# Performance work log

Measured on AMD Instinct MI355X. Metric: run time of the kernel, lower is better.

Reference implementation:

```python
import jax, jax.numpy as jnp
import numpy as np

D_MODEL = 1024
N_HEADS = 16
D_K = 64

def setup_inputs() -> dict:
    key = jax.random.key(0)
    k0, k1, k2, k3, k4 = jax.random.split(key, 5)
    B, S = 4, 4096
    std = 0.02
    x = jax.random.normal(k0, (B, S, D_MODEL), dtype=jnp.float32)
    # nn.Linear weights are [out, in]; init normal(0, 0.02) as in _init_weights
    W_q = std * jax.random.normal(k1, (N_HEADS * D_K, D_MODEL), dtype=jnp.float32)
    W_k = std * jax.random.normal(k2, (N_HEADS * D_K, D_MODEL), dtype=jnp.float32)
    W_v = std * jax.random.normal(k3, (N_HEADS * D_K, D_MODEL), dtype=jnp.float32)
    W_o = std * jax.random.normal(k4, (D_MODEL, N_HEADS * D_K), dtype=jnp.float32)
    return {"x": x, "W_q": W_q, "W_k": W_k, "W_v": W_v, "W_o": W_o}

def reference(x, W_q, W_k, W_v, W_o):
    B, S, _ = x.shape
    H, Dk = N_HEADS, D_K
    # projections (nn.Linear: x @ W.T), reshape to [B, S, H, Dk]
    q = (x @ W_q.T).reshape(B, S, H, Dk)
    k = (x @ W_k.T).reshape(B, S, H, Dk)
    v = (x @ W_v.T).reshape(B, S, H, Dk)
    scale = 1.0 / jnp.sqrt(jnp.float32(Dk))
    # No softmax between the two matmuls -> reassociate (QK^T)V = Q(K^TV),
    # identical math, O(S*d^2) instead of O(S^2*d).
    kv = jnp.einsum('bshd,bshe->bhde', k, v)          # [B, H, Dk, Dk]
    attn = jnp.einsum('bshd,bhde->bshe', q, kv) * scale  # [B, S, H, Dk]
    out = attn.reshape(B, S, H * Dk) @ W_o.T
    return out
```

## Files before the change

kernel.cpp:

```cpp
#include <hip/hip_runtime.h>
#include <hip/hip_bf16.h>
#include <cstdint>


typedef __bf16 bf16x8 __attribute__((ext_vector_type(8)));
typedef float f32x4 __attribute__((ext_vector_type(4)));
typedef unsigned short ushort_t;

__device__ inline void gld_lds16(const void* g, void* l) {
    __builtin_amdgcn_global_load_lds(
        (const __attribute__((address_space(1))) unsigned int*)g,
        (__attribute__((address_space(3))) unsigned int*)l,
        16, 0, 0);
}

__device__ inline ushort_t f2bf(float f) {
    uint32_t u = __float_as_uint(f);
    uint32_t r = (u + 0x7fffu + ((u >> 16) & 1u)) >> 16;
    return (ushort_t)r;
}
__device__ inline float bf2f(ushort_t u) {
    return __uint_as_float((uint32_t)u << 16);
}

template <typename OutT>
__global__ __launch_bounds__(256, 2)
void gemm_bt(const ushort_t* __restrict__ A, int lda, long strideA,
             const ushort_t* __restrict__ B, int ldb, long strideB,
             OutT* __restrict__ C0, int ldc0, long strideC0, int K)
{
    __shared__ ushort_t lA[128 * 32];
    __shared__ ushort_t lB[128 * 32];

    const int t    = threadIdx.x;
    const int lane = t & 63;
    const int wid  = t >> 6;
    const int z    = blockIdx.z;

    A += (size_t)z * strideA;
    B += (size_t)z * strideB;

    const int m0 = blockIdx.x * 128;
    const int n0 = blockIdx.y * 128;

    const int wm = (wid >> 1) * 64;
    const int wn = (wid & 1) * 64;
    const int mr = lane & 15;
    const int q4 = lane >> 4;

    const int row_a = t >> 2;
    const int seg   = ((t & 3) ^ ((t >> 3) & 3)) * 8;
    const int csw   = (q4 ^ ((mr >> 1) & 3)) * 16;

    f32x4 acc[4][4] = {};

    for (int k0 = 0; k0 < K; k0 += 32) {
        __syncthreads();
        gld_lds16(A + (size_t)(m0 + row_a) * lda + k0 + seg,      (char*)lA + wid * 1024);
        gld_lds16(A + (size_t)(m0 + 64 + row_a) * lda + k0 + seg, (char*)lA + 4096 + wid * 1024);
        gld_lds16(B + (size_t)(n0 + row_a) * ldb + k0 + seg,      (char*)lB + wid * 1024);
        gld_lds16(B + (size_t)(n0 + 64 + row_a) * ldb + k0 + seg, (char*)lB + 4096 + wid * 1024);
        __syncthreads();

        bf16x8 af[4], bf[4];
#pragma unroll
        for (int i = 0; i < 4; ++i)
            af[i] = *(const bf16x8*)((const char*)lA + (wm + i * 16 + mr) * 64 + csw);
#pragma unroll
        for (int j = 0; j < 4; ++j)
            bf[j] = *(const bf16x8*)((const char*)lB + (wn + j * 16 + mr) * 64 + csw);
#pragma unroll
        for (int i = 0; i < 4; ++i)
#pragma unroll
            for (int j = 0; j < 4; ++j)
                acc[i][j] = __builtin_amdgcn_mfma_f32_16x16x32_bf16(af[i], bf[j], acc[i][j], 0, 0, 0);
    }

    OutT* Cw = C0 + (size_t)z * strideC0;
#pragma unroll
    for (int i = 0; i < 4; ++i) {
        const int rbase = m0 + wm + i * 16 + q4 * 4;
#pragma unroll
        for (int j = 0; j < 4; ++j) {
            const int col = n0 + wn + j * 16 + mr;
#pragma unroll
            for (int r = 0; r < 4; ++r) {
                const float v = acc[i][j][r];
                const size_t off = (size_t)(rbase + r) * ldc0 + col;
                if constexpr (sizeof(OutT) == 2) Cw[off] = f2bf(v);
                else                             Cw[off] = v;
            }
        }
    }
}

__global__ __launch_bounds__(256, 2)
void gemm_gram(const ushort_t* __restrict__ X, ushort_t* __restrict__ Gp)
{
    __shared__ ushort_t lA[128 * 32];
    __shared__ ushort_t lB[128 * 32];

    const int t    = threadIdx.x;
    const int lane = t & 63;
    const int wid  = t >> 6;

    const int z  = blockIdx.x;
    const int bb = z >> 2, ks = z & 3;

    int ti = 0, rem = blockIdx.y;
    while (rem >= 8 - ti) { rem -= 8 - ti; ++ti; }
    const int tj = ti + rem;
    const int m0 = ti * 128;
    const int n0 = tj * 128;

    const ushort_t* A = X + (size_t)bb * 4096 + (size_t)ks * 1024;

    const int wm = (wid >> 1) * 64;
    const int wn = (wid & 1) * 64;
    const int mr = lane & 15;
    const int q4 = lane >> 4;

    const int row_a = t >> 2;
    const int seg   = ((t & 3) ^ ((t >> 3) & 3)) * 8;
    const int csw   = (q4 ^ ((mr >> 1) & 3)) * 16;

    f32x4 acc[4][4] = {};

    for (int k0 = 0; k0 < 1024; k0 += 32) {
        __syncthreads();
        gld_lds16(A + (size_t)(m0 + row_a) * 16384 + k0 + seg,      (char*)lA + wid * 1024);
        gld_lds16(A + (size_t)(m0 + 64 + row_a) * 16384 + k0 + seg, (char*)lA + 4096 + wid * 1024);
        gld_lds16(A + (size_t)(n0 + row_a) * 16384 + k0 + seg,      (char*)lB + wid * 1024);
        gld_lds16(A + (size_t)(n0 + 64 + row_a) * 16384 + k0 + seg, (char*)lB + 4096 + wid * 1024);
        __syncthreads();

        bf16x8 af[4], bf[4];
#pragma unroll
        for (int i = 0; i < 4; ++i)
            af[i] = *(const bf16x8*)((const char*)lA + (wm + i * 16 + mr) * 64 + csw);
#pragma unroll
        for (int j = 0; j < 4; ++j)
            bf[j] = *(const bf16x8*)((const char*)lB + (wn + j * 16 + mr) * 64 + csw);
#pragma unroll
        for (int i = 0; i < 4; ++i)
#pragma unroll
            for (int j = 0; j < 4; ++j)
                acc[i][j] = __builtin_amdgcn_mfma_f32_16x16x32_bf16(af[i], bf[j], acc[i][j], 0, 0, 0);
    }

    ushort_t* Cw = Gp + ((size_t)z << 20);
#pragma unroll
    for (int i = 0; i < 4; ++i) {
        const int rbase = m0 + wm + i * 16 + q4 * 4;
#pragma unroll
        for (int j = 0; j < 4; ++j) {
            const int col = n0 + wn + j * 16 + mr;
#pragma unroll
            for (int r = 0; r < 4; ++r)
                Cw[(size_t)(rbase + r) * 1024 + col] = f2bf(acc[i][j][r]);
        }
    }
}

__global__ __launch_bounds__(256)
void reduce_g_t(const ushort_t* __restrict__ Gp, ushort_t* __restrict__ G)
{
    __shared__ float acc[64 * 65];

    const int t  = threadIdx.x;
    const int b  = blockIdx.y;
    const int tr = blockIdx.x >> 4, tc = blockIdx.x & 15;
    const int sr = (tr <= tc) ? tr : tc;
    const int sc = (tr <= tc) ? tc : tr;
    const bool flip = tr > tc;

#pragma unroll
    for (int p = 0; p < 4; ++p) {
        const int idx = p * 256 + t;
        const int r = idx >> 4, c = (idx & 15) * 4;
        float a0 = 0.f, a1 = 0.f, a2 = 0.f, a3 = 0.f;
#pragma unroll
        for (int ksl = 0; ksl < 4; ++ksl) {
            const ushort4 u = *(const ushort4*)&Gp[((size_t)(b * 4 + ksl) << 20)
                                                   + (size_t)(sr * 64 + r) * 1024 + sc * 64 + c];
            a0 += bf2f(u.x); a1 += bf2f(u.y); a2 += bf2f(u.z); a3 += bf2f(u.w);
        }
        acc[r * 65 + c + 0] = a0;
        acc[r * 65 + c + 1] = a1;
        acc[r * 65 + c + 2] = a2;
        acc[r * 65 + c + 3] = a3;
    }
    __syncthreads();

#pragma unroll
    for (int p = 0; p < 4; ++p) {
        const int idx = p * 256 + t;
        const int r = idx >> 4, c = (idx & 15) * 4;
        float v0, v1, v2, v3;
        if (flip) {
            v0 = acc[(c + 0) * 65 + r];
            v1 = acc[(c + 1) * 65 + r];
            v2 = acc[(c + 2) * 65 + r];
            v3 = acc[(c + 3) * 65 + r];
        } else {
            v0 = acc[r * 65 + c + 0];
            v1 = acc[r * 65 + c + 1];
            v2 = acc[r * 65 + c + 2];
            v3 = acc[r * 65 + c + 3];
        }
        ushort4 o;
        o.x = f2bf(v0); o.y = f2bf(v1); o.z = f2bf(v2); o.w = f2bf(v3);
        *(ushort4*)&G[((size_t)b << 20) + (size_t)(tr * 64 + r) * 1024 + tc * 64 + c] = o;
    }
}

__global__ __launch_bounds__(256)
void cast_x_t(const float* __restrict__ x, ushort_t* __restrict__ xb,
              ushort_t* __restrict__ xbT)
{
    __shared__ ushort_t lt[64 * 66];
    const int t  = threadIdx.x;
    const int s0 = blockIdx.x * 64;
    const int i0 = blockIdx.y * 64;

#pragma unroll
    for (int c = 0; c < 4; ++c) {
        const int idx = c * 256 + t;
        const int r = idx >> 4, c4 = (idx & 15) * 4;
        const float4 f = *(const float4*)&x[(size_t)(s0 + r) * 1024 + i0 + c4];
        ushort4 o;
        o.x = f2bf(f.x); o.y = f2bf(f.y); o.z = f2bf(f.z); o.w = f2bf(f.w);
        *(ushort4*)&xb[(size_t)(s0 + r) * 1024 + i0 + c4] = o;
        *(uint32_t*)&lt[r * 66 + c4]     = (uint32_t)o.x | ((uint32_t)o.y << 16);
        *(uint32_t*)&lt[r * 66 + c4 + 2] = (uint32_t)o.z | ((uint32_t)o.w << 16);
    }
    __syncthreads();
#pragma unroll
    for (int c = 0; c < 4; ++c) {
        const int idx = c * 256 + t;
        const int ri = idx >> 4, s4 = (idx & 15) * 4;
        ushort4 o;
        o.x = lt[(s4 + 0) * 66 + ri];
        o.y = lt[(s4 + 1) * 66 + ri];
        o.z = lt[(s4 + 2) * 66 + ri];
        o.w = lt[(s4 + 3) * 66 + ri];
        *(ushort4*)&xbT[(size_t)(i0 + ri) * 16384 + s0 + s4] = o;
    }
}

__global__ __launch_bounds__(256)
void cast_wt(const float* __restrict__ W, ushort_t* __restrict__ WT)
{
    __shared__ ushort_t lt[64 * 66];
    const int t  = threadIdx.x;
    const int r0 = blockIdx.x * 64;
    const int c0 = blockIdx.y * 64;

#pragma unroll
    for (int c = 0; c < 4; ++c) {
        const int idx = c * 256 + t;
        const int r = idx >> 4, c4 = (idx & 15) * 4;
        const float4 f = *(const float4*)&W[(size_t)(r0 + r) * 1024 + c0 + c4];
        ushort4 o;
        o.x = f2bf(f.x); o.y = f2bf(f.y); o.z = f2bf(f.z); o.w = f2bf(f.w);
        *(uint32_t*)&lt[r * 66 + c4]     = (uint32_t)o.x | ((uint32_t)o.y << 16);
        *(uint32_t*)&lt[r * 66 + c4 + 2] = (uint32_t)o.z | ((uint32_t)o.w << 16);
    }
    __syncthreads();
#pragma unroll
    for (int c = 0; c < 4; ++c) {
        const int idx = c * 256 + t;
        const int ri = idx >> 4, s4 = (idx & 15) * 4;
        ushort4 o;
        o.x = lt[(s4 + 0) * 66 + ri];
        o.y = lt[(s4 + 1) * 66 + ri];
        o.z = lt[(s4 + 2) * 66 + ri];
        o.w = lt[(s4 + 3) * 66 + ri];
        *(ushort4*)&WT[(size_t)(c0 + ri) * 1024 + r0 + s4] = o;
    }
}

__global__ __launch_bounds__(256)
void cast_w2(const float* __restrict__ a, const float* __restrict__ b,
             ushort_t* __restrict__ out)
{
    const float* src = (blockIdx.y == 0) ? a : b;
    const int i = (blockIdx.x * 256 + threadIdx.x) * 4;
    const float4 f = *(const float4*)&src[i];
    ushort4 o;
    o.x = f2bf(f.x); o.y = f2bf(f.y); o.z = f2bf(f.z); o.w = f2bf(f.w);
    *(ushort4*)&out[(size_t)blockIdx.y * 1048576 + i] = o;
}

__global__ __launch_bounds__(256)
void kvblk(const ushort_t* __restrict__ H, const ushort_t* __restrict__ Wv,
           float* __restrict__ KVp)
{
    __shared__ ushort_t sH[64 * 132];
    __shared__ ushort_t sV[64 * 132];

    const int t  = threadIdx.x;
    const int is = blockIdx.x;
    const int bh = blockIdx.y;
    const int b  = bh >> 4, h = bh & 15;

    const ushort_t* Hp = H + ((size_t)b << 20) + (size_t)(h * 64) * 1024 + is * 128;
    const ushort_t* Vp = Wv + (size_t)(h * 64) * 1024 + is * 128;

#pragma unroll
    for (int i2 = 0; i2 < 8; ++i2) {
        const int ci = i2 * 256 + t;
        const int r = ci >> 5, c = (ci & 31) * 4;
        *(uint2*)&sH[r * 132 + c] = *(const uint2*)&Hp[(size_t)r * 1024 + c];
        *(uint2*)&sV[r * 132 + c] = *(const uint2*)&Vp[(size_t)r * 1024 + c];
    }
    __syncthreads();

    const int d0 = (t >> 4) * 4;
    const int e0 = (t & 15) * 4;
    float acc[4][4] = {};

#pragma unroll 2
    for (int i4 = 0; i4 < 128; i4 += 4) {
        uint2 hu[4], vu[4];
#pragma unroll
        for (int j = 0; j < 4; ++j) {
            hu[j] = *(const uint2*)&sH[(d0 + j) * 132 + i4];
            vu[j] = *(const uint2*)&sV[(e0 + j) * 132 + i4];
        }
        float hf[4][4], vf[4][4];
#pragma unroll
        for (int j = 0; j < 4; ++j) {
            hf[j][0] = __uint_as_float(hu[j].x << 16);
            hf[j][1] = __uint_as_float(hu[j].x & 0xffff0000u);
            hf[j][2] = __uint_as_float(hu[j].y << 16);
            hf[j][3] = __uint_as_float(hu[j].y & 0xffff0000u);
            vf[j][0] = __uint_as_float(vu[j].x << 16);
            vf[j][1] = __uint_as_float(vu[j].x & 0xffff0000u);
            vf[j][2] = __uint_as_float(vu[j].y << 16);
            vf[j][3] = __uint_as_float(vu[j].y & 0xffff0000u);
        }
#pragma unroll
        for (int ii = 0; ii < 4; ++ii)
#pragma unroll
            for (int di = 0; di < 4; ++di)
#pragma unroll
                for (int ej = 0; ej < 4; ++ej)
                    acc[di][ej] += hf[di][ii] * vf[ej][ii];
    }

    float* outp = KVp + ((size_t)(is * 64 + bh)) * 4096;
#pragma unroll
    for (int i = 0; i < 4; ++i) {
        float4 o; o.x = acc[i][0]; o.y = acc[i][1]; o.z = acc[i][2]; o.w = acc[i][3];
        *(float4*)&outp[(d0 + i) * 64 + e0] = o;
    }
}

__global__ __launch_bounds__(256)
void reduce_kv8(const float4* __restrict__ in, float4* __restrict__ out)
{
    const int i = blockIdx.x * 256 + threadIdx.x;
    float4 a = in[i];
#pragma unroll
    for (int s = 1; s < 8; ++s) {
        const float4 b = in[s * 65536 + i];
        a.x += b.x; a.y += b.y; a.z += b.z; a.w += b.w;
    }
    out[i] = a;
}

__global__ __launch_bounds__(256)
void make_E(const float* __restrict__ KV, const float* __restrict__ Wo,
            ushort_t* __restrict__ Et)
{
    __shared__ float skv[64 * 65];
    __shared__ float swo[64 * 65];

    const int t  = threadIdx.x;
    const int bh = blockIdx.y;
    const int b  = bh >> 4, h = bh & 15;
    const int j0 = blockIdx.x * 64;

    const float* kvp = KV + (size_t)bh * 4096;
#pragma unroll
    for (int i = 0; i < 4; ++i) {
        const int idx = t + i * 256;
        const int r = idx >> 4, c = (idx & 15) * 4;
        const float4 f = *(const float4*)&kvp[r * 64 + c];
        skv[r * 65 + c + 0] = f.x;
        skv[r * 65 + c + 1] = f.y;
        skv[r * 65 + c + 2] = f.z;
        skv[r * 65 + c + 3] = f.w;
        const float4 g = *(const float4*)&Wo[(size_t)(j0 + r) * 1024 + h * 64 + c];
        swo[r * 65 + c + 0] = g.x;
        swo[r * 65 + c + 1] = g.y;
        swo[r * 65 + c + 2] = g.z;
        swo[r * 65 + c + 3] = g.w;
    }
    __syncthreads();

    const int d0 = (t & 15) * 4;
#pragma unroll
    for (int pass = 0; pass < 4; ++pass) {
        const int jloc = (t >> 4) + pass * 16;
        float s0 = 0.f, s1 = 0.f, s2 = 0.f, s3 = 0.f;
        const float* wrow = &swo[jloc * 65];
#pragma unroll 8
        for (int e = 0; e < 64; ++e) {
            const float w = wrow[e];
            s0 += skv[(d0 + 0) * 65 + e] * w;
            s1 += skv[(d0 + 1) * 65 + e] * w;
            s2 += skv[(d0 + 2) * 65 + e] * w;
            s3 += skv[(d0 + 3) * 65 + e] * w;
        }
        ushort4 o;
        o.x = f2bf(s0 * 0.125f);
        o.y = f2bf(s1 * 0.125f);
        o.z = f2bf(s2 * 0.125f);
        o.w = f2bf(s3 * 0.125f);
        *(ushort4*)&Et[((size_t)b * 1024 + j0 + jloc) * 1024 + h * 64 + d0] = o;
    }
}


extern "C" void kernel_launch(void* const* d_in, const int* in_sizes, int n_in,
                              void* d_out, int out_size, void* d_ws, size_t ws_size,
                              hipStream_t stream)
{
    const float* x  = (const float*)d_in[0];
    const float* Wq = (const float*)d_in[1];
    const float* Wk = (const float*)d_in[2];
    const float* Wv = (const float*)d_in[3];
    const float* Wo = (const float*)d_in[4];
    float* out = (float*)d_out;

    const int B = 4, S = 4096, D = 1024;
    const long MB1 = 1048576;

    char* ws = (char*)d_ws;
    size_t off = 0;
    auto alloc = [&](size_t bytes) -> void* {
        void* p = ws + off;
        off += (bytes + 255) & ~(size_t)255;
        return p;
    };
    ushort_t* xb   = (ushort_t*)alloc((size_t)B * S * D * 2);
    ushort_t* xbT  = (ushort_t*)alloc((size_t)D * B * S * 2);
    ushort_t* wkv  = (ushort_t*)alloc((size_t)2 * D * D * 2);
    ushort_t* wqT  = (ushort_t*)alloc((size_t)D * D * 2);
    ushort_t* Gb   = (ushort_t*)alloc((size_t)B * D * D * 2);
    float*    kvp  = (float*)alloc((size_t)8 * 64 * 4096 * 4);
    float*    kvr  = (float*)alloc((size_t)64 * 4096 * 4);
    ushort_t* Fb   = (ushort_t*)alloc((size_t)B * D * D * 2);
    char*     R1   = (char*)alloc((size_t)16 * MB1 * 2);
    ushort_t* Gp = (ushort_t*)R1;
    ushort_t* Hb = (ushort_t*)R1;
    ushort_t* Et = (ushort_t*)(R1 + 8 * MB1 * 2);
    ushort_t* wkb = wkv;
    ushort_t* wvb = wkv + MB1;

    cast_x_t<<<dim3(256, 16), dim3(256), 0, stream>>>(x, xb, xbT);
    cast_w2<<<dim3(1024, 2), dim3(256), 0, stream>>>(Wk, Wv, wkv);
    cast_wt<<<dim3(16, 16), dim3(256), 0, stream>>>(Wq, wqT);

    gemm_gram<<<dim3(16, 36), dim3(256), 0, stream>>>(xbT, Gp);
    reduce_g_t<<<dim3(256, 4), dim3(256), 0, stream>>>(Gp, Gb);

    gemm_bt<ushort_t><<<dim3(8, 8, 4), dim3(256), 0, stream>>>(
        wkb, D, 0, Gb, D, MB1, Hb, D, MB1, D);

    kvblk<<<dim3(8, 64), dim3(256), 0, stream>>>(Hb, wvb, kvp);
    reduce_kv8<<<dim3(256), dim3(256), 0, stream>>>((const float4*)kvp, (float4*)kvr);

    make_E<<<dim3(16, 64), dim3(256), 0, stream>>>(kvr, Wo, Et);

    gemm_bt<ushort_t><<<dim3(8, 8, 4), dim3(256), 0, stream>>>(
        Et, D, MB1, wqT, D, 0, Fb, D, (long)D * D, D);

    gemm_bt<float><<<dim3(32, 8, 4), dim3(256), 0, stream>>>(
        xb, D, (long)S * D, Fb, D, (long)D * D, out, D, (long)S * D, D);
}
```

Measured before the change: 315.9 us.

## Add 256x256-tile pipelined GEMM kernel for the final output projection

Replaces the 128x128-tile final GEMM (x @ F per batch, fp32 output) with a new 512-thread kernel using 256x256 tiles, 64-wide K steps, double-buffered LDS fed by direct global-to-LDS loads, XOR-swizzled layout, and staging interleaved with MFMA phases under manual waitcnt/barrier control. The larger tile raises arithmetic intensity and cuts global/LDS traffic per flop, and the interleaved prefetch is meant to hide load latency. The cost is 128KB of LDS per block, which limits occupancy. Only 256 blocks are launched, so part of the GPU may sit idle.

Measured after the change: 307.8 us. 2.6% less time.

```diff
diff --git a/kernel.cpp b/kernel.cpp
--- a/kernel.cpp
+++ b/kernel.cpp
@@ -90,6 +90,124 @@
                 if constexpr (sizeof(OutT) == 2) Cw[off] = f2bf(v);
                 else                             Cw[off] = v;
             }
+        }
+    }
+}
+
+__global__ __launch_bounds__(512, 2)
+void gemm256_bt(const ushort_t* __restrict__ A, int lda, long strideA,
+                const ushort_t* __restrict__ B, int ldb, long strideB,
+                float* __restrict__ C, int ldc, long strideC, int K)
+{
+    __shared__ char lds[131072];
+
+    const int t    = threadIdx.x;
+    const int lane = t & 63;
+    const int wid  = t >> 6;
+    const int z    = blockIdx.z;
+
+    A += (size_t)z * strideA;
+    B += (size_t)z * strideB;
+
+    const int m0 = blockIdx.x * 256;
+    const int n0 = blockIdx.y * 256;
+
+    const int wm = wid >> 2;
+    const int wn = wid & 3;
+    const int mr = lane & 15;
+    const int q4 = lane >> 4;
+
+    const int NT = K >> 6;
+
+    const int srow = t >> 3;
+    const int scol = ((t & 7) << 3) ^ (((t >> 3) & 7) << 3);
+
+    auto stage_half = [&](const ushort_t* __restrict__ src, int ld, int org,
+                          int h, int tgt, int bsel) {
+        if (tgt >= NT) return;
+        char* base = lds + bsel + ((tgt & 1) << 15) + (h << 14) + wid * 1024;
+        const ushort_t* g = src + (size_t)(org + h * 128 + srow) * ld + tgt * 64 + scol;
+        gld_lds16(g, base);
+        gld_lds16(g + ((size_t)ld << 6), base + 8192);
+    };
+    auto stage_unit = [&](int u, int tgt) {
+        if (u < 2) stage_half(B, ldb, n0, u,     tgt, 65536);
+        else       stage_half(A, lda, m0, u - 2, tgt, 0);
+    };
+
+    stage_unit(0, 0); stage_unit(1, 0); stage_unit(2, 0); stage_unit(3, 0);
+    stage_unit(0, 1); stage_unit(1, 1); stage_unit(2, 1);
+    asm volatile("s_waitcnt vmcnt(6)" ::: "memory");
+    __builtin_amdgcn_s_barrier();
+
+    f32x4 acc[8][4] = {};
+
+    for (int kt = 0; kt < NT; ++kt) {
+        const char* aBuf = lds + ((kt & 1) << 15) + (wm << 14);
+        const char* bBuf = lds + 65536 + ((kt & 1) << 15) + ((wn >> 1) << 14);
+        const int cb = (wn & 1) << 6;
+
+        bf16x8 bB[4][2];
+#pragma unroll
+        for (int p = 0; p < 4; ++p) {
+            bf16x8 aA[2][2];
+#pragma unroll
+            for (int s = 0; s < 2; ++s) {
+                const int lr = (2 * p + s) * 16 + mr;
+                const int kx = (lr & 7) << 4;
+#pragma unroll
+                for (int ks = 0; ks < 2; ++ks)
+                    aA[s][ks] = *(const bf16x8*)(aBuf + lr * 128 + ((ks * 64 + q4 * 16) ^ kx));
+            }
+            if (p == 0) {
+#pragma unroll
+                for (int j = 0; j < 4; ++j) {
+                    const int c  = cb + j * 16 + mr;
+                    const int kx = (c & 7) << 4;
+#pragma unroll
+                    for (int ks = 0; ks < 2; ++ks)
+                        bB[j][ks] = *(const bf16x8*)(bBuf + c * 128 + ((ks * 64 + q4 * 16) ^ kx));
+                }
+            }
+            if      (p == 0) stage_unit(3, kt + 1);
+            else if (p == 1) stage_unit(0, kt + 2);
+            else if (p == 2) stage_unit(1, kt + 2);
+            else             stage_unit(2, kt + 2);
+
+            __builtin_amdgcn_s_barrier();
+            asm volatile("s_waitcnt lgkmcnt(0)" ::: "memory");
+            __builtin_amdgcn_sched_barrier(0);
+
+            __builtin_amdgcn_s_setprio(1);
+#pragma unroll
+            for (int s = 0; s < 2; ++s)
+#pragma unroll
+                for (int j = 0; j < 4; ++j)
+#pragma unroll
+                    for (int ks = 0; ks < 2; ++ks)
+                        acc[2 * p + s][j] = __builtin_amdgcn_mfma_f32_16x16x32_bf16(
+                            aA[s][ks], bB[j][ks], acc[2 * p + s][j], 0, 0, 0);
+            __builtin_amdgcn_s_setprio(0);
+            __builtin_amdgcn_sched_barrier(0);
+
+            if (p == 3) {
+                if (kt == NT - 2)     asm volatile("s_waitcnt vmcnt(0)" ::: "memory");
+                else if (kt < NT - 2) asm volatile("s_waitcnt vmcnt(6)" ::: "memory");
+            }
+            __builtin_amdgcn_s_barrier();
+        }
+    }
+
+    float* Cw = C + (size_t)z * strideC;
+#pragma unroll
+    for (int i = 0; i < 8; ++i) {
+        const int row = m0 + wm * 128 + i * 16 + q4 * 4;
+#pragma unroll
+        for (int j = 0; j < 4; ++j) {
+            const int col = n0 + wn * 64 + j * 16 + mr;
+#pragma unroll
+            for (int r = 0; r < 4; ++r)
+                Cw[(size_t)(row + r) * ldc + col] = acc[i][j][r];
         }
     }
 }
@@ -478,6 +596,6 @@
     gemm_bt<ushort_t><<<dim3(8, 8, 4), dim3(256), 0, stream>>>(
         Et, D, MB1, wqT, D, 0, Fb, D, (long)D * D, D);
 
-    gemm_bt<float><<<dim3(32, 8, 4), dim3(256), 0, stream>>>(
+    gemm256_bt<<<dim3(16, 4, 4), dim3(512), 0, stream>>>(
         xb, D, (long)S * D, Fb, D, (long)D * D, out, D, (long)S * D, D);
 }
```

## Triple-buffer LDS pipelines for gram and final GEMMs, halve N tile for mid GEMMs

Applied to the files above, without the earlier changes.

Replaces the synchronous load-then-compute loops of the gram GEMM and the final output GEMM with a 3-stage LDS ring. Global-to-LDS loads are issued two tiles ahead and gated by vmcnt waits plus raw barriers, with setprio around the MFMA block. The final GEMM moves to a 256x128 tile with 8x4 accumulators per wave to raise reuse. The two 1024x1024 batched GEMMs switch to 128x64 tiles so the grid has twice as many blocks for better CU occupancy. The cost is more LDS and register pressure and hand-managed wait counts that must match the number of loads issued per stage.

Result: no change. 313.9 us (-0.6%).

```diff
diff --git a/kernel.cpp b/kernel.cpp
--- a/kernel.cpp
+++ b/kernel.cpp
@@ -24,13 +24,13 @@
 }
 
 template <typename OutT>
-__global__ __launch_bounds__(256, 2)
-void gemm_bt(const ushort_t* __restrict__ A, int lda, long strideA,
-             const ushort_t* __restrict__ B, int ldb, long strideB,
-             OutT* __restrict__ C0, int ldc0, long strideC0, int K)
+__global__ __launch_bounds__(256, 4)
+void gemm_bt_n64(const ushort_t* __restrict__ A, int lda, long strideA,
+                 const ushort_t* __restrict__ B, int ldb, long strideB,
+                 OutT* __restrict__ C0, int ldc0, long strideC0, int K)
 {
     __shared__ ushort_t lA[128 * 32];
-    __shared__ ushort_t lB[128 * 32];
+    __shared__ ushort_t lB[64 * 32];
 
     const int t    = threadIdx.x;
     const int lane = t & 63;
@@ -41,10 +41,10 @@
     B += (size_t)z * strideB;
 
     const int m0 = blockIdx.x * 128;
-    const int n0 = blockIdx.y * 128;
+    const int n0 = blockIdx.y * 64;
 
     const int wm = (wid >> 1) * 64;
-    const int wn = (wid & 1) * 64;
+    const int wn = (wid & 1) * 32;
     const int mr = lane & 15;
     const int q4 = lane >> 4;
 
@@ -52,27 +52,26 @@
     const int seg   = ((t & 3) ^ ((t >> 3) & 3)) * 8;
     const int csw   = (q4 ^ ((mr >> 1) & 3)) * 16;
 
-    f32x4 acc[4][4] = {};
+    f32x4 acc[4][2] = {};
 
     for (int k0 = 0; k0 < K; k0 += 32) {
         __syncthreads();
         gld_lds16(A + (size_t)(m0 + row_a) * lda + k0 + seg,      (char*)lA + wid * 1024);
         gld_lds16(A + (size_t)(m0 + 64 + row_a) * lda + k0 + seg, (char*)lA + 4096 + wid * 1024);
         gld_lds16(B + (size_t)(n0 + row_a) * ldb + k0 + seg,      (char*)lB + wid * 1024);
-        gld_lds16(B + (size_t)(n0 + 64 + row_a) * ldb + k0 + seg, (char*)lB + 4096 + wid * 1024);
         __syncthreads();
 
-        bf16x8 af[4], bf[4];
+        bf16x8 af[4], bf[2];
 #pragma unroll
         for (int i = 0; i < 4; ++i)
             af[i] = *(const bf16x8*)((const char*)lA + (wm + i * 16 + mr) * 64 + csw);
 #pragma unroll
-        for (int j = 0; j < 4; ++j)
+        for (int j = 0; j < 2; ++j)
             bf[j] = *(const bf16x8*)((const char*)lB + (wn + j * 16 + mr) * 64 + csw);
 #pragma unroll
         for (int i = 0; i < 4; ++i)
 #pragma unroll
-            for (int j = 0; j < 4; ++j)
+            for (int j = 0; j < 2; ++j)
                 acc[i][j] = __builtin_amdgcn_mfma_f32_16x16x32_bf16(af[i], bf[j], acc[i][j], 0, 0, 0);
     }
 
@@ -81,7 +80,7 @@
     for (int i = 0; i < 4; ++i) {
         const int rbase = m0 + wm + i * 16 + q4 * 4;
 #pragma unroll
-        for (int j = 0; j < 4; ++j) {
+        for (int j = 0; j < 2; ++j) {
             const int col = n0 + wn + j * 16 + mr;
 #pragma unroll
             for (int r = 0; r < 4; ++r) {
@@ -95,10 +94,104 @@
 }
 
 __global__ __launch_bounds__(256, 2)
-void gemm_gram(const ushort_t* __restrict__ X, ushort_t* __restrict__ Gp)
-{
-    __shared__ ushort_t lA[128 * 32];
-    __shared__ ushort_t lB[128 * 32];
+void gemm_fin(const ushort_t* __restrict__ A, int lda, long strideA,
+              const ushort_t* __restrict__ B, int ldb, long strideB,
+              float* __restrict__ C, int ldc, long strideC, int K)
+{
+    __shared__ char lds[73728];
+
+    const int t    = threadIdx.x;
+    const int lane = t & 63;
+    const int wid  = t >> 6;
+    const int z    = blockIdx.z;
+
+    A += (size_t)z * strideA;
+    B += (size_t)z * strideB;
+
+    const int m0 = blockIdx.x * 256;
+    const int n0 = blockIdx.y * 128;
+
+    const int wr = wid >> 1;
+    const int wn = wid & 1;
+    const int mr = lane & 15;
+    const int q4 = lane >> 4;
+
+    const int NT = K >> 5;
+
+    const int row_a = t >> 2;
+    const int seg   = ((t & 3) ^ ((t >> 3) & 3)) * 8;
+    const int csw   = (q4 ^ ((mr >> 1) & 3)) * 16;
+
+    auto stage = [&](int tgt, int bsel) {
+        if (tgt >= NT) return;
+        char* base = lds + bsel * 24576 + wid * 1024;
+        const ushort_t* gA = A + (size_t)(m0 + row_a) * lda + tgt * 32 + seg;
+        gld_lds16(gA,                          base);
+        gld_lds16(gA + ((size_t)lda << 6),     base + 4096);
+        gld_lds16(gA + ((size_t)lda << 7),     base + 8192);
+        gld_lds16(gA + (size_t)lda * 192,      base + 12288);
+        const ushort_t* gB = B + (size_t)(n0 + row_a) * ldb + tgt * 32 + seg;
+        gld_lds16(gB,                          base + 16384);
+        gld_lds16(gB + ((size_t)ldb << 6),     base + 20480);
+    };
+
+    bf16x8 af[8], bf[4];
+    f32x4 acc[8][4] = {};
+
+    stage(0, 0);
+    stage(1, 1);
+    asm volatile("s_waitcnt vmcnt(6)" ::: "memory");
+    __builtin_amdgcn_s_barrier();
+
+    int cur = 0;
+    for (int kt = 0; kt < NT; ++kt) {
+        const char* buf = lds + cur * 24576;
+#pragma unroll
+        for (int i = 0; i < 8; ++i)
+            af[i] = *(const bf16x8*)(buf + (wr * 128 + i * 16 + mr) * 64 + csw);
+#pragma unroll
+        for (int j = 0; j < 4; ++j)
+            bf[j] = *(const bf16x8*)(buf + 16384 + (wn * 64 + j * 16 + mr) * 64 + csw);
+
+        int b2 = cur + 2; if (b2 >= 3) b2 -= 3;
+        stage(kt + 2, b2);
+
+        asm volatile("s_waitcnt lgkmcnt(0)" ::: "memory");
+        __builtin_amdgcn_sched_barrier(0);
+        __builtin_amdgcn_s_setprio(1);
+#pragma unroll
+        for (int i = 0; i < 8; ++i)
+#pragma unroll
+            for (int j = 0; j < 4; ++j)
+                acc[i][j] = __builtin_amdgcn_mfma_f32_16x16x32_bf16(
+                    af[i], bf[j], acc[i][j], 0, 0, 0);
+        __builtin_amdgcn_s_setprio(0);
+        __builtin_amdgcn_sched_barrier(0);
+
+        if (kt + 2 < NT)       asm volatile("s_waitcnt vmcnt(6)" ::: "memory");
+        else if (kt + 2 == NT) asm volatile("s_waitcnt vmcnt(0)" ::: "memory");
+        __builtin_amdgcn_s_barrier();
+        if (++cur == 3) cur = 0;
+    }
+
+    float* Cw = C + (size_t)z * strideC;
+#pragma unroll
+    for (int i = 0; i < 8; ++i) {
+        const int rbase = m0 + wr * 128 + i * 16 + q4 * 4;
+#pragma unroll
+        for (int j = 0; j < 4; ++j) {
+            const int col = n0 + wn * 64 + j * 16 + mr;
+#pragma unroll
+            for (int r = 0; r < 4; ++r)
+                Cw[(size_t)(rbase + r) * ldc + col] = acc[i][j][r];
+        }
+    }
+}
+
+__global__ __launch_bounds__(256, 3)
+void gemm_gram3(const ushort_t* __restrict__ X, ushort_t* __restrict__ Gp)
+{
+    __shared__ char lds[49152];
 
     const int t    = threadIdx.x;
     const int lane = t & 63;
@@ -114,6 +207,7 @@
     const int n0 = tj * 128;
 
     const ushort_t* A = X + (size_t)bb * 4096 + (size_t)ks * 1024;
+    const int NT = 32;
 
     const int wm = (wid >> 1) * 64;
     const int wn = (wid & 1) * 64;
@@ -124,28 +218,54 @@
     const int seg   = ((t & 3) ^ ((t >> 3) & 3)) * 8;
     const int csw   = (q4 ^ ((mr >> 1) & 3)) * 16;
 
+    auto stage = [&](int tgt, int bsel) {
+        if (tgt >= NT) return;
+        char* base = lds + bsel * 16384 + wid * 1024;
+        const ushort_t* gA = A + (size_t)(m0 + row_a) * 16384 + tgt * 32 + seg;
+        gld_lds16(gA,                       base);
+        gld_lds16(gA + ((size_t)16384 << 6), base + 4096);
+        const ushort_t* gB = A + (size_t)(n0 + row_a) * 16384 + tgt * 32 + seg;
+        gld_lds16(gB,                       base + 8192);
+        gld_lds16(gB + ((size_t)16384 << 6), base + 12288);
+    };
+
+    bf16x8 af[4], bf[4];
     f32x4 acc[4][4] = {};
 
-    for (int k0 = 0; k0 < 1024; k0 += 32) {
-        __syncthreads();
-        gld_lds16(A + (size_t)(m0 + row_a) * 16384 + k0 + seg,      (char*)lA + wid * 1024);
-        gld_lds16(A + (size_t)(m0 + 64 + row_a) * 16384 + k0 + seg, (char*)lA + 4096 + wid * 1024);
-        gld_lds16(A + (size_t)(n0 + row_a) * 16384 + k0 + seg,      (char*)lB + wid * 1024);
-        gld_lds16(A + (size_t)(n0 + 64 + row_a) * 16384 + k0 + seg, (char*)lB + 4096 + wid * 1024);
-        __syncthreads();
-
-        bf16x8 af[4], bf[4];
+    stage(0, 0);
+    stage(1, 1);
+    asm volatile("s_waitcnt vmcnt(4)" ::: "memory");
+    __builtin_amdgcn_s_barrier();
+
+    int cur = 0;
+    for (int kt = 0; kt < NT; ++kt) {
+        const char* buf = lds + cur * 16384;
 #pragma unroll
         for (int i = 0; i < 4; ++i)
-            af[i] = *(const bf16x8*)((const char*)lA + (wm + i * 16 + mr) * 64 + csw);
+            af[i] = *(const bf16x8*)(buf + (wm + i * 16 + mr) * 64 + csw);
 #pragma unroll
         for (int j = 0; j < 4; ++j)
-            bf[j] = *(const bf16x8*)((const char*)lB + (wn + j * 16 + mr) * 64 + csw);
+            bf[j] = *(const bf16x8*)(buf + 8192 + (wn + j * 16 + mr) * 64 + csw);
+
+        int b2 = cur + 2; if (b2 >= 3) b2 -= 3;
+        stage(kt + 2, b2);
+
+        asm volatile("s_waitcnt lgkmcnt(0)" ::: "memory");
+        __builtin_amdgcn_sched_barrier(0);
+        __builtin_amdgcn_s_setprio(1);
 #pragma unroll
         for (int i = 0; i < 4; ++i)
 #pragma unroll
             for (int j = 0; j < 4; ++j)
-                acc[i][j] = __builtin_amdgcn_mfma_f32_16x16x32_bf16(af[i], bf[j], acc[i][j], 0, 0, 0);
+                acc[i][j] = __builtin_amdgcn_mfma_f32_16x16x32_bf16(
+                    af[i], bf[j], acc[i][j], 0, 0, 0);
+        __builtin_amdgcn_s_setprio(0);
+        __builtin_amdgcn_sched_barrier(0);
+
+        if (kt + 2 < NT)       asm volatile("s_waitcnt vmcnt(4)" ::: "memory");
+        else if (kt + 2 == NT) asm volatile("s_waitcnt vmcnt(0)" ::: "memory");
+        __builtin_amdgcn_s_barrier();
+        if (++cur == 3) cur = 0;
     }
 
     ushort_t* Cw = Gp + ((size_t)z << 20);
@@ -464,10 +584,10 @@
     cast_w2<<<dim3(1024, 2), dim3(256), 0, stream>>>(Wk, Wv, wkv);
     cast_wt<<<dim3(16, 16), dim3(256), 0, stream>>>(Wq, wqT);
 
-    gemm_gram<<<dim3(16, 36), dim3(256), 0, stream>>>(xbT, Gp);
+    gemm_gram3<<<dim3(16, 36), dim3(256), 0, stream>>>(xbT, Gp);
     reduce_g_t<<<dim3(256, 4), dim3(256), 0, stream>>>(Gp, Gb);
 
-    gemm_bt<ushort_t><<<dim3(8, 8, 4), dim3(256), 0, stream>>>(
+    gemm_bt_n64<ushort_t><<<dim3(8, 16, 4), dim3(256), 0, stream>>>(
         wkb, D, 0, Gb, D, MB1, Hb, D, MB1, D);
 
     kvblk<<<dim3(8, 64), dim3(256), 0, stream>>>(Hb, wvb, kvp);
@@ -475,9 +595,9 @@
 
     make_E<<<dim3(16, 64), dim3(256), 0, stream>>>(kvr, Wo, Et);
 
-    gemm_bt<ushort_t><<<dim3(8, 8, 4), dim3(256), 0, stream>>>(
+    gemm_bt_n64<ushort_t><<<dim3(8, 16, 4), dim3(256), 0, stream>>>(
         Et, D, MB1, wqT, D, 0, Fb, D, (long)D * D, D);
 
-    gemm_bt<float><<<dim3(32, 8, 4), dim3(256), 0, stream>>>(
+    gemm_fin<<<dim3(16, 8, 4), dim3(256), 0, stream>>>(
         xb, D, (long)S * D, Fb, D, (long)D * D, out, D, (long)S * D, D);
 }
```
